# Performance work log

Hardware: AMD Instinct MI355X
Metric: run time of the kernel (lower is better)

Reference implementation:

```python
import jax, jax.numpy as jnp
import numpy as np

N, E, B = 100000, 1600000, 64
IN, HID, OUT, ED = 64, 128, 128, 2
K, ALPHA = 16, 0.1
LN_EPS = 1e-5


def setup_inputs() -> dict:
    key = jax.random.key(0)
    ks = jax.random.split(key, 24)
    def gl(k, shape, fan_in):
        return jax.random.uniform(k, shape, jnp.float32, -1.0, 1.0) / np.sqrt(fan_in)
    inp = {
        "x": jax.random.normal(ks[0], (N, IN), jnp.float32),
        "edge_index": jax.random.randint(ks[1], (2, E), 0, N, jnp.int64),
        "batch": jnp.sort(jax.random.randint(ks[2], (N,), 0, B, jnp.int64)),
        "edge_attr": jax.random.normal(ks[3], (E, ED), jnp.float32),
        # conv1: edge lin (ED->IN) + mlp (IN->HID->HID)
        "We1": gl(ks[4], (ED, IN), ED), "be1": jnp.zeros((IN,)),
        "W1a": gl(ks[5], (IN, HID), IN), "b1a": jnp.zeros((HID,)),
        "W1b": gl(ks[6], (HID, HID), HID), "b1b": jnp.zeros((HID,)),
        "g1": jnp.ones((HID,)), "bn1": jnp.zeros((HID,)),
        # conv2: edge lin (ED->HID) + mlp (HID->OUT->OUT)
        "We2": gl(ks[7], (ED, HID), ED), "be2": jnp.zeros((HID,)),
        "W2a": gl(ks[8], (HID, OUT), HID), "b2a": jnp.zeros((OUT,)),
        "W2b": gl(ks[9], (OUT, OUT), OUT), "b2b": jnp.zeros((OUT,)),
        "g2": jnp.ones((OUT,)), "bn2": jnp.zeros((OUT,)),
        # gate nn (OUT -> OUT//2 -> 1)
        "Wg1": gl(ks[10], (OUT, OUT // 2), OUT), "bg1": jnp.zeros((OUT // 2,)),
        "Wg2": gl(ks[11], (OUT // 2, 1), OUT // 2), "bg2": jnp.zeros((1,)),
    }
    return inp


def _gelu(x):
    return jax.nn.gelu(x, approximate=False)


def _layernorm(x, g, b):
    mu = jnp.mean(x, axis=-1, keepdims=True)
    var = jnp.mean(jnp.square(x - mu), axis=-1, keepdims=True)
    return (x - mu) * jax.lax.rsqrt(var + LN_EPS) * g + b


def _gine(x, src, dst, edge_attr, We, be, W1, b1, W2, b2):
    # message: ReLU(x_j + lin(edge_attr)), aggregated by sum at dst; eps=0
    m = jax.nn.relu(x[src] + edge_attr @ We + be)          # [E, d]
    agg = jax.ops.segment_sum(m, dst, num_segments=N)      # [N, d]
    h = x + agg
    return _gelu(h @ W1 + b1) @ W2 + b2


def _appnp(x, src, dst):
    # gcn_norm with self-loops: deg_i = 1 + in-degree
    deg = jax.ops.segment_sum(jnp.ones((E,), x.dtype), dst, num_segments=N) + 1.0
    dis = jax.lax.rsqrt(deg)
    w = dis[src] * dis[dst]            # [E]
    selfw = 1.0 / deg                  # [N]
    def step(i, h):
        prop = jax.ops.segment_sum(w[:, None] * h[src], dst, num_segments=N) \
               + selfw[:, None] * h
        return (1.0 - ALPHA) * prop + ALPHA * x
    return jax.lax.fori_loop(0, K, step, x)


def reference(x, edge_index, batch, edge_attr,
              We1, be1, W1a, b1a, W1b, b1b, g1, bn1,
              We2, be2, W2a, b2a, W2b, b2b, g2, bn2,
              Wg1, bg1, Wg2, bg2):
    src, dst = edge_index[0], edge_index[1]
    h = _gine(x, src, dst, edge_attr, We1, be1, W1a, b1a, W1b, b1b)
    h = _layernorm(_gelu(h), g1, bn1)
    # dropout is identity in eval
    h = _gine(h, src, dst, edge_attr, We2, be2, W2a, b2a, W2b, b2b)
    h = _layernorm(h, g2, bn2)
    h = _appnp(h, src, dst)
    # attentional aggregation: per-graph softmax over gate scores
    gate = (_gelu(h @ Wg1 + bg1) @ Wg2 + bg2)[:, 0]        # [N]
    m = jax.ops.segment_max(gate, batch, num_segments=B)    # [B]
    e = jnp.exp(gate - m[batch])
    s = jax.ops.segment_sum(e, batch, num_segments=B)
    a = e / s[batch]
    g = jax.ops.segment_sum(a[:, None] * h, batch, num_segments=B)  # [B, OUT]
    return h, g
```

## Files before the change

kernel.cpp:

```cpp
#include <hip/hip_runtime.h>
#include <math.h>

#define N_NODES 100000
#define N_EDGES 1600000
#define N_B 64
#define D_IN 64
#define D_HID 128
#define D_OUT 128
#define K_ITER 16
#define LN_EPS 1e-5f

typedef short s8v __attribute__((ext_vector_type(8)));
typedef float f4v __attribute__((ext_vector_type(4)));

__device__ __forceinline__ float gelu_f(float x) {
    return 0.5f * x * (1.0f + erff(0.70710678118654752440f * x));
}

__device__ __forceinline__ float ubx(unsigned u) { return __uint_as_float(u << 16); }
__device__ __forceinline__ float uby(unsigned u) { return __uint_as_float(u & 0xffff0000u); }

__device__ __forceinline__ unsigned short bf_rne(float x) {
    unsigned u = __float_as_uint(x);
    u += 0x7fffu + ((u >> 16) & 1u);
    return (unsigned short)(u >> 16);
}
__device__ __forceinline__ float bf_f(unsigned short s) {
    return __uint_as_float(((unsigned)s) << 16);
}
__device__ __forceinline__ unsigned pack_bf2(float a, float b) {
    return (unsigned)bf_rne(a) | (((unsigned)bf_rne(b)) << 16);
}


__global__ __launch_bounds__(256) void hist_kernel(const int* __restrict__ dst, int* __restrict__ counts) {
    int e = blockIdx.x * 256 + threadIdx.x;
    if (e < N_EDGES) atomicAdd(&counts[dst[e]], 1);
}

__global__ __launch_bounds__(256) void deg_kernel(const int* __restrict__ counts,
                                                  float* __restrict__ dis, float* __restrict__ selfw) {
    int i = blockIdx.x * 256 + threadIdx.x;
    if (i < N_NODES) {
        float d = (float)(counts[i] + 1);
        dis[i] = 1.0f / sqrtf(d);
        selfw[i] = 1.0f / d;
    }
}

__global__ __launch_bounds__(1024) void scan1(const int* __restrict__ counts, int* __restrict__ rp,
                                              int* __restrict__ bsum) {
    __shared__ int tmp[1024];
    int t = threadIdx.x;
    int idx = blockIdx.x * 1024 + t;
    int v = (idx < N_NODES) ? counts[idx] : 0;
    tmp[t] = v;
    __syncthreads();
    for (int o = 1; o < 1024; o <<= 1) {
        int add = (t >= o) ? tmp[t - o] : 0;
        __syncthreads();
        tmp[t] += add;
        __syncthreads();
    }
    if (idx < N_NODES) rp[idx] = tmp[t] - v;
    if (t == 1023) bsum[blockIdx.x] = tmp[t];
}

__global__ void scan2(int* bsum, int nb) {
    if (threadIdx.x == 0 && blockIdx.x == 0) {
        int acc = 0;
        for (int i = 0; i < nb; i++) { int v = bsum[i]; bsum[i] = acc; acc += v; }
    }
}

__global__ __launch_bounds__(1024) void scan3(int* __restrict__ rp, const int* __restrict__ bsum,
                                              int* __restrict__ cursor) {
    int t = threadIdx.x;
    int idx = blockIdx.x * 1024 + t;
    if (idx < N_NODES) {
        int v = rp[idx] + bsum[blockIdx.x];
        rp[idx] = v;
        cursor[idx] = v;
    }
    if (idx == 0) rp[N_NODES] = N_EDGES;
}

__global__ __launch_bounds__(256) void scatter_kernel(const int* __restrict__ src, const int* __restrict__ dst,
                                                      const float* __restrict__ ea, const float* __restrict__ dis,
                                                      int* __restrict__ cursor, int2* __restrict__ esw,
                                                      float2* __restrict__ eea) {
    int e = blockIdx.x * 256 + threadIdx.x;
    if (e >= N_EDGES) return;
    int s = src[e], d = dst[e];
    int pos = atomicAdd(&cursor[d], 1);
    int2 sw;
    sw.x = s;
    sw.y = __float_as_int(dis[s] * dis[d]);
    esw[pos] = sw;
    float2 e2;
    e2.x = ea[e * 2];
    e2.y = ea[e * 2 + 1];
    eea[pos] = e2;
}


__global__ __launch_bounds__(256) void conv1_gather(const float* __restrict__ x, const int* __restrict__ rp,
                                                    const int2* __restrict__ esw, const float2* __restrict__ eea,
                                                    const float* __restrict__ We1, const float* __restrict__ be1,
                                                    float* __restrict__ out) {
    int gw = (blockIdx.x * 256 + threadIdx.x) >> 6;
    if (gw >= N_NODES) return;
    int lane = threadIdx.x & 63;
    float w0 = We1[lane], w1 = We1[64 + lane], bb = be1[lane];
    float acc = x[(size_t)gw * 64 + lane];
    int j = rp[gw], s1 = rp[gw + 1];
    for (; j + 4 <= s1; j += 4) {
        int2 e0 = esw[j], e1 = esw[j + 1], e2 = esw[j + 2], e3 = esw[j + 3];
        float2 a0 = eea[j], a1 = eea[j + 1], a2 = eea[j + 2], a3 = eea[j + 3];
        float v0 = x[(size_t)e0.x * 64 + lane];
        float v1 = x[(size_t)e1.x * 64 + lane];
        float v2 = x[(size_t)e2.x * 64 + lane];
        float v3 = x[(size_t)e3.x * 64 + lane];
        acc += fmaxf(v0 + a0.x * w0 + a0.y * w1 + bb, 0.0f);
        acc += fmaxf(v1 + a1.x * w0 + a1.y * w1 + bb, 0.0f);
        acc += fmaxf(v2 + a2.x * w0 + a2.y * w1 + bb, 0.0f);
        acc += fmaxf(v3 + a3.x * w0 + a3.y * w1 + bb, 0.0f);
    }
    for (; j < s1; j++) {
        int2 e = esw[j];
        float2 a = eea[j];
        float v = x[(size_t)e.x * 64 + lane];
        acc += fmaxf(v + a.x * w0 + a.y * w1 + bb, 0.0f);
    }
    out[(size_t)gw * 64 + lane] = acc;
}

__global__ __launch_bounds__(256) void conv2_gather(const float* __restrict__ h1f, const unsigned* __restrict__ h1b,
                                                    const int* __restrict__ rp,
                                                    const int2* __restrict__ esw, const float2* __restrict__ eea,
                                                    const float* __restrict__ We2, const float* __restrict__ be2,
                                                    float* __restrict__ out) {
    int gw = (blockIdx.x * 256 + threadIdx.x) >> 6;
    if (gw >= N_NODES) return;
    int lane = threadIdx.x & 63;
    int f0 = lane * 2;
    float w00 = We2[f0], w01 = We2[f0 + 1];
    float w10 = We2[128 + f0], w11 = We2[128 + f0 + 1];
    float b0 = be2[f0], b1 = be2[f0 + 1];
    float2 hc = ((const float2*)h1f)[(size_t)gw * 64 + lane];
    float a0 = hc.x, a1 = hc.y;
    int j = rp[gw], s1 = rp[gw + 1];
    for (; j + 8 <= s1; j += 8) {
        int2 e0 = esw[j], e1 = esw[j + 1], e2 = esw[j + 2], e3 = esw[j + 3];
        int2 e4 = esw[j + 4], e5 = esw[j + 5], e6 = esw[j + 6], e7 = esw[j + 7];
        float2 q0 = eea[j], q1 = eea[j + 1], q2 = eea[j + 2], q3 = eea[j + 3];
        float2 q4 = eea[j + 4], q5 = eea[j + 5], q6 = eea[j + 6], q7 = eea[j + 7];
        unsigned v0 = h1b[(size_t)e0.x * 64 + lane];
        unsigned v1 = h1b[(size_t)e1.x * 64 + lane];
        unsigned v2 = h1b[(size_t)e2.x * 64 + lane];
        unsigned v3 = h1b[(size_t)e3.x * 64 + lane];
        unsigned v4 = h1b[(size_t)e4.x * 64 + lane];
        unsigned v5 = h1b[(size_t)e5.x * 64 + lane];
        unsigned v6 = h1b[(size_t)e6.x * 64 + lane];
        unsigned v7 = h1b[(size_t)e7.x * 64 + lane];
        a0 += fmaxf(ubx(v0) + q0.x * w00 + q0.y * w10 + b0, 0.0f);
        a1 += fmaxf(uby(v0) + q0.x * w01 + q0.y * w11 + b1, 0.0f);
        a0 += fmaxf(ubx(v1) + q1.x * w00 + q1.y * w10 + b0, 0.0f);
        a1 += fmaxf(uby(v1) + q1.x * w01 + q1.y * w11 + b1, 0.0f);
        a0 += fmaxf(ubx(v2) + q2.x * w00 + q2.y * w10 + b0, 0.0f);
        a1 += fmaxf(uby(v2) + q2.x * w01 + q2.y * w11 + b1, 0.0f);
        a0 += fmaxf(ubx(v3) + q3.x * w00 + q3.y * w10 + b0, 0.0f);
        a1 += fmaxf(uby(v3) + q3.x * w01 + q3.y * w11 + b1, 0.0f);
        a0 += fmaxf(ubx(v4) + q4.x * w00 + q4.y * w10 + b0, 0.0f);
        a1 += fmaxf(uby(v4) + q4.x * w01 + q4.y * w11 + b1, 0.0f);
        a0 += fmaxf(ubx(v5) + q5.x * w00 + q5.y * w10 + b0, 0.0f);
        a1 += fmaxf(uby(v5) + q5.x * w01 + q5.y * w11 + b1, 0.0f);
        a0 += fmaxf(ubx(v6) + q6.x * w00 + q6.y * w10 + b0, 0.0f);
        a1 += fmaxf(uby(v6) + q6.x * w01 + q6.y * w11 + b1, 0.0f);
        a0 += fmaxf(ubx(v7) + q7.x * w00 + q7.y * w10 + b0, 0.0f);
        a1 += fmaxf(uby(v7) + q7.x * w01 + q7.y * w11 + b1, 0.0f);
    }
    for (; j < s1; j++) {
        int2 e = esw[j];
        float2 q = eea[j];
        unsigned v = h1b[(size_t)e.x * 64 + lane];
        a0 += fmaxf(ubx(v) + q.x * w00 + q.y * w10 + b0, 0.0f);
        a1 += fmaxf(uby(v) + q.x * w01 + q.y * w11 + b1, 0.0f);
    }
    out[(size_t)gw * 128 + f0] = a0;
    out[(size_t)gw * 128 + f0 + 1] = a1;
}


template <int Kd, bool GELU, bool LN, int OMODE>
__global__ __launch_bounds__(256) void mlp_mfma(const float* __restrict__ A, const float* __restrict__ W,
                                                const float* __restrict__ bias, const float* __restrict__ g,
                                                const float* __restrict__ bn, float* __restrict__ outf,
                                                unsigned short* __restrict__ outb) {
    __shared__ unsigned short sHi[8192];
    __shared__ unsigned short sLo[8192];
    int wave = threadIdx.x >> 6, lane = threadIdx.x & 63;
    int quad = lane >> 4, n = lane & 15;
    int rowA = blockIdx.x * 64 + wave * 16 + n;
    int rowAc = (rowA < N_NODES) ? rowA : 0;

    f4v acc[8];
    #pragma unroll
    for (int t = 0; t < 8; t++) acc[t] = (f4v){0.f, 0.f, 0.f, 0.f};

    for (int ph = 0; ph < Kd / 64; ph++) {
        __syncthreads();
        for (int idx = threadIdx.x; idx < 8192; idx += 256) {
            int k = idx >> 7, c = idx & 127;
            float v = W[(size_t)(ph * 64 + k) * 128 + c];
            unsigned short hi = bf_rne(v);
            unsigned short lo = bf_rne(v - bf_f(hi));
            int kk = k >> 5, q = (k >> 3) & 3, j = k & 7, t = c >> 4, nn = c & 15;
            int lidx = ((((kk * 4 + q) * 8 + t) * 16 + nn) << 3) + j;
            sHi[lidx] = hi;
            sLo[lidx] = lo;
        }
        __syncthreads();
        #pragma unroll
        for (int kk = 0; kk < 2; kk++) {
            int k0 = ph * 64 + kk * 32 + quad * 8;
            const float4* ap = (const float4*)(A + (size_t)rowAc * Kd + k0);
            float4 a0 = ap[0], a1 = ap[1];
            float av[8] = {a0.x, a0.y, a0.z, a0.w, a1.x, a1.y, a1.z, a1.w};
            s8v ahi, alo;
            #pragma unroll
            for (int j = 0; j < 8; j++) {
                unsigned short h = bf_rne(av[j]);
                ahi[j] = (short)h;
                alo[j] = (short)bf_rne(av[j] - bf_f(h));
            }
            int base = ((kk * 4 + quad) * 8) * 128;
            #pragma unroll
            for (int t = 0; t < 8; t++) {
                s8v bhi = *(const s8v*)&sHi[base + ((t * 16 + n) << 3)];
                s8v blo = *(const s8v*)&sLo[base + ((t * 16 + n) << 3)];
                acc[t] = __builtin_amdgcn_mfma_f32_16x16x32_bf16(ahi, bhi, acc[t], 0, 0, 0);
                acc[t] = __builtin_amdgcn_mfma_f32_16x16x32_bf16(ahi, blo, acc[t], 0, 0, 0);
                acc[t] = __builtin_amdgcn_mfma_f32_16x16x32_bf16(alo, bhi, acc[t], 0, 0, 0);
            }
        }
    }

    float bcol[8], gcol[8], bncol[8];
    #pragma unroll
    for (int t = 0; t < 8; t++) {
        bcol[t] = bias[t * 16 + n];
        if (LN) { gcol[t] = g[t * 16 + n]; bncol[t] = bn[t * 16 + n]; }
    }
    #pragma unroll
    for (int r = 0; r < 4; r++) {
        int row = blockIdx.x * 64 + wave * 16 + quad * 4 + r;
        float v[8];
        #pragma unroll
        for (int t = 0; t < 8; t++) {
            float x = acc[t][r] + bcol[t];
            v[t] = GELU ? gelu_f(x) : x;
        }
        if (LN) {
            float s = 0.f, q2 = 0.f;
            #pragma unroll
            for (int t = 0; t < 8; t++) { s += v[t]; q2 += v[t] * v[t]; }
            #pragma unroll
            for (int m = 1; m <= 8; m <<= 1) {
                s += __shfl_xor(s, m, 64);
                q2 += __shfl_xor(q2, m, 64);
            }
            float mu = s * (1.0f / 128.0f);
            float rs = rsqrtf(q2 * (1.0f / 128.0f) - mu * mu + LN_EPS);
            #pragma unroll
            for (int t = 0; t < 8; t++) v[t] = (v[t] - mu) * rs * gcol[t] + bncol[t];
        }
        if (row < N_NODES) {
            #pragma unroll
            for (int t = 0; t < 8; t++) {
                if (OMODE != 2) outf[(size_t)row * 128 + t * 16 + n] = v[t];
                if (OMODE >= 1) outb[(size_t)row * 128 + t * 16 + n] = bf_rne(v[t]);
            }
        }
    }
}


__global__ __launch_bounds__(256) void gate_mfma(const float* __restrict__ h, const float* __restrict__ Wg1,
                                                 const float* __restrict__ bg1, const float* __restrict__ Wg2,
                                                 const float* __restrict__ bg2, float* __restrict__ gate) {
    __shared__ unsigned short sHi[8192];
    __shared__ unsigned short sLo[8192];
    int wave = threadIdx.x >> 6, lane = threadIdx.x & 63;
    int quad = lane >> 4, n = lane & 15;
    for (int idx = threadIdx.x; idx < 8192; idx += 256) {
        int k = idx >> 6, c = idx & 63;
        float v = Wg1[k * 64 + c];
        unsigned short hi = bf_rne(v);
        unsigned short lo = bf_rne(v - bf_f(hi));
        int kk = k >> 5, q = (k >> 3) & 3, j = k & 7, t = c >> 4, nn = c & 15;
        int lidx = ((((kk * 4 + q) * 4 + t) * 16 + nn) << 3) + j;
        sHi[lidx] = hi;
        sLo[lidx] = lo;
    }
    __syncthreads();
    int rowA = blockIdx.x * 64 + wave * 16 + n;
    int rowAc = (rowA < N_NODES) ? rowA : 0;
    f4v acc[4];
    #pragma unroll
    for (int t = 0; t < 4; t++) acc[t] = (f4v){0.f, 0.f, 0.f, 0.f};
    #pragma unroll
    for (int kk = 0; kk < 4; kk++) {
        const float4* ap = (const float4*)(h + (size_t)rowAc * 128 + kk * 32 + quad * 8);
        float4 a0 = ap[0], a1 = ap[1];
        float av[8] = {a0.x, a0.y, a0.z, a0.w, a1.x, a1.y, a1.z, a1.w};
        s8v ahi, alo;
        #pragma unroll
        for (int j = 0; j < 8; j++) {
            unsigned short hh = bf_rne(av[j]);
            ahi[j] = (short)hh;
            alo[j] = (short)bf_rne(av[j] - bf_f(hh));
        }
        int base = ((kk * 4 + quad) * 4) * 128;
        #pragma unroll
        for (int t = 0; t < 4; t++) {
            s8v bhi = *(const s8v*)&sHi[base + ((t * 16 + n) << 3)];
            s8v blo = *(const s8v*)&sLo[base + ((t * 16 + n) << 3)];
            acc[t] = __builtin_amdgcn_mfma_f32_16x16x32_bf16(ahi, bhi, acc[t], 0, 0, 0);
            acc[t] = __builtin_amdgcn_mfma_f32_16x16x32_bf16(ahi, blo, acc[t], 0, 0, 0);
            acc[t] = __builtin_amdgcn_mfma_f32_16x16x32_bf16(alo, bhi, acc[t], 0, 0, 0);
        }
    }
    float b2 = bg2[0];
    float bb[4], vv[4];
    #pragma unroll
    for (int t = 0; t < 4; t++) { bb[t] = bg1[t * 16 + n]; vv[t] = Wg2[t * 16 + n]; }
    #pragma unroll
    for (int r = 0; r < 4; r++) {
        int row = blockIdx.x * 64 + wave * 16 + quad * 4 + r;
        float val = 0.f;
        #pragma unroll
        for (int t = 0; t < 4; t++) val += gelu_f(acc[t][r] + bb[t]) * vv[t];
        #pragma unroll
        for (int m = 1; m <= 8; m <<= 1) val += __shfl_xor(val, m, 64);
        if (n == 0 && row < N_NODES) gate[row] = val + b2;
    }
}


template <bool LAST>
__global__ __launch_bounds__(256) void appnp_step_bf(const unsigned* __restrict__ hin,
                                                     const unsigned* __restrict__ anchor,
                                                     unsigned* __restrict__ hout, float2* __restrict__ houtf,
                                                     const int* __restrict__ rp, const int2* __restrict__ esw,
                                                     const float* __restrict__ selfw) {
    int gw = (blockIdx.x * 256 + threadIdx.x) >> 6;
    if (gw >= N_NODES) return;
    int lane = threadIdx.x & 63;
    size_t idx = (size_t)gw * 64 + lane;
    float swi = selfw[gw];
    unsigned hcp = hin[idx];
    float ax = swi * ubx(hcp), ay = swi * uby(hcp);
    int j = rp[gw], s1 = rp[gw + 1];
    for (; j + 8 <= s1; j += 8) {
        int2 e0 = esw[j], e1 = esw[j + 1], e2 = esw[j + 2], e3 = esw[j + 3];
        int2 e4 = esw[j + 4], e5 = esw[j + 5], e6 = esw[j + 6], e7 = esw[j + 7];
        unsigned v0 = hin[(size_t)e0.x * 64 + lane];
        unsigned v1 = hin[(size_t)e1.x * 64 + lane];
        unsigned v2 = hin[(size_t)e2.x * 64 + lane];
        unsigned v3 = hin[(size_t)e3.x * 64 + lane];
        unsigned v4 = hin[(size_t)e4.x * 64 + lane];
        unsigned v5 = hin[(size_t)e5.x * 64 + lane];
        unsigned v6 = hin[(size_t)e6.x * 64 + lane];
        unsigned v7 = hin[(size_t)e7.x * 64 + lane];
        float w0 = __int_as_float(e0.y), w1 = __int_as_float(e1.y);
        float w2 = __int_as_float(e2.y), w3 = __int_as_float(e3.y);
        float w4 = __int_as_float(e4.y), w5 = __int_as_float(e5.y);
        float w6 = __int_as_float(e6.y), w7 = __int_as_float(e7.y);
        ax = fmaf(w0, ubx(v0), ax); ay = fmaf(w0, uby(v0), ay);
        ax = fmaf(w1, ubx(v1), ax); ay = fmaf(w1, uby(v1), ay);
        ax = fmaf(w2, ubx(v2), ax); ay = fmaf(w2, uby(v2), ay);
        ax = fmaf(w3, ubx(v3), ax); ay = fmaf(w3, uby(v3), ay);
        ax = fmaf(w4, ubx(v4), ax); ay = fmaf(w4, uby(v4), ay);
        ax = fmaf(w5, ubx(v5), ax); ay = fmaf(w5, uby(v5), ay);
        ax = fmaf(w6, ubx(v6), ax); ay = fmaf(w6, uby(v6), ay);
        ax = fmaf(w7, ubx(v7), ax); ay = fmaf(w7, uby(v7), ay);
    }
    for (; j + 4 <= s1; j += 4) {
        int2 e0 = esw[j], e1 = esw[j + 1], e2 = esw[j + 2], e3 = esw[j + 3];
        unsigned v0 = hin[(size_t)e0.x * 64 + lane];
        unsigned v1 = hin[(size_t)e1.x * 64 + lane];
        unsigned v2 = hin[(size_t)e2.x * 64 + lane];
        unsigned v3 = hin[(size_t)e3.x * 64 + lane];
        float w0 = __int_as_float(e0.y), w1 = __int_as_float(e1.y);
        float w2 = __int_as_float(e2.y), w3 = __int_as_float(e3.y);
        ax = fmaf(w0, ubx(v0), ax); ay = fmaf(w0, uby(v0), ay);
        ax = fmaf(w1, ubx(v1), ax); ay = fmaf(w1, uby(v1), ay);
        ax = fmaf(w2, ubx(v2), ax); ay = fmaf(w2, uby(v2), ay);
        ax = fmaf(w3, ubx(v3), ax); ay = fmaf(w3, uby(v3), ay);
    }
    for (; j < s1; j++) {
        int2 e = esw[j];
        unsigned v = hin[(size_t)e.x * 64 + lane];
        float w = __int_as_float(e.y);
        ax = fmaf(w, ubx(v), ax); ay = fmaf(w, uby(v), ay);
    }
    unsigned ancp = anchor[idx];
    float ox = 0.9f * ax + 0.1f * ubx(ancp);
    float oy = 0.9f * ay + 0.1f * uby(ancp);
    if (LAST) {
        float2 o; o.x = ox; o.y = oy;
        houtf[idx] = o;
    } else {
        hout[idx] = pack_bf2(ox, oy);
    }
}


__global__ void seg_begin(const int* __restrict__ batch, int* __restrict__ gbeg) {
    int b = threadIdx.x;
    if (b > N_B) return;
    if (b == N_B) { gbeg[N_B] = N_NODES; return; }
    int lo = 0, hi = N_NODES;
    while (lo < hi) {
        int mid = (lo + hi) >> 1;
        if (batch[mid] < b) lo = mid + 1; else hi = mid;
    }
    gbeg[b] = lo;
}

__global__ __launch_bounds__(256) void seg_max(const float* __restrict__ gate, const int* __restrict__ gbeg,
                                               float* __restrict__ gmax) {
    int b = blockIdx.x;
    int s = gbeg[b], e = gbeg[b + 1];
    float m = -INFINITY;
    for (int i = s + threadIdx.x; i < e; i += 256) m = fmaxf(m, gate[i]);
    for (int o = 32; o > 0; o >>= 1) m = fmaxf(m, __shfl_xor(m, o, 64));
    __shared__ float red[4];
    if ((threadIdx.x & 63) == 0) red[threadIdx.x >> 6] = m;
    __syncthreads();
    if (threadIdx.x == 0) gmax[b] = fmaxf(fmaxf(red[0], red[1]), fmaxf(red[2], red[3]));
}

__global__ __launch_bounds__(256) void seg_sum(const float* __restrict__ gate, const int* __restrict__ gbeg,
                                               const float* __restrict__ gmax, float* __restrict__ gsum) {
    int b = blockIdx.x;
    int s = gbeg[b], e = gbeg[b + 1];
    float m = gmax[b];
    float acc = 0.0f;
    for (int i = s + threadIdx.x; i < e; i += 256) acc += expf(gate[i] - m);
    for (int o = 32; o > 0; o >>= 1) acc += __shfl_xor(acc, o, 64);
    __shared__ float red[4];
    if ((threadIdx.x & 63) == 0) red[threadIdx.x >> 6] = acc;
    __syncthreads();
    if (threadIdx.x == 0) gsum[b] = red[0] + red[1] + red[2] + red[3];
}

__global__ __launch_bounds__(512) void seg_pool(const float* __restrict__ h, const float* __restrict__ gate,
                                                const int* __restrict__ gbeg, const float* __restrict__ gmax,
                                                const float* __restrict__ gsum, float* __restrict__ gout) {
    int b = blockIdx.x >> 3, slice = blockIdx.x & 7;
    int team = threadIdx.x >> 7;
    int f = threadIdx.x & 127;
    int s = gbeg[b], e = gbeg[b + 1];
    float m = gmax[b];
    float inv = (e > s) ? 1.0f / gsum[b] : 0.0f;
    float acc = 0.0f;
    for (int i = s + slice * 4 + team; i < e; i += 32) {
        float a = expf(gate[i] - m) * inv;
        acc = fmaf(a, h[(size_t)i * 128 + f], acc);
    }
    __shared__ float red[4][128];
    red[team][f] = acc;
    __syncthreads();
    if (team == 0) {
        float v = red[0][f] + red[1][f] + red[2][f] + red[3][f];
        atomicAdd(&gout[b * 128 + f], v);
    }
}


extern "C" void kernel_launch(void* const* d_in, const int* in_sizes, int n_in,
                              void* d_out, int out_size, void* d_ws, size_t ws_size,
                              hipStream_t stream) {
    const float* x     = (const float*)d_in[0];
    const int*   ei    = (const int*)d_in[1];
    const int*   batch = (const int*)d_in[2];
    const float* ea    = (const float*)d_in[3];
    const float* We1 = (const float*)d_in[4];
    const float* be1 = (const float*)d_in[5];
    const float* W1a = (const float*)d_in[6];
    const float* b1a = (const float*)d_in[7];
    const float* W1b = (const float*)d_in[8];
    const float* b1b = (const float*)d_in[9];
    const float* g1  = (const float*)d_in[10];
    const float* bn1 = (const float*)d_in[11];
    const float* We2 = (const float*)d_in[12];
    const float* be2 = (const float*)d_in[13];
    const float* W2a = (const float*)d_in[14];
    const float* b2a = (const float*)d_in[15];
    const float* W2b = (const float*)d_in[16];
    const float* b2b = (const float*)d_in[17];
    const float* g2  = (const float*)d_in[18];
    const float* bn2 = (const float*)d_in[19];
    const float* Wg1 = (const float*)d_in[20];
    const float* bg1 = (const float*)d_in[21];
    const float* Wg2 = (const float*)d_in[22];
    const float* bg2 = (const float*)d_in[23];

    float* outH = (float*)d_out;
    float* outG = outH + (size_t)N_NODES * 128;

    char* w = (char*)d_ws;
    auto carve = [&](size_t bytes) {
        void* p = (void*)w;
        w += ((bytes + 255) / 256) * 256;
        return p;
    };
    float*  bufB   = (float*)carve((size_t)N_NODES * 128 * 4);
    float*  bufC   = (float*)carve((size_t)N_NODES * 128 * 4);
    int2*   esw    = (int2*)carve((size_t)N_EDGES * 8);
    float2* eea    = (float2*)carve((size_t)N_EDGES * 8);
    int*    counts = (int*)carve((size_t)N_NODES * 4);
    int*    rp     = (int*)carve((size_t)(N_NODES + 1) * 4);
    int*    cursor = (int*)carve((size_t)N_NODES * 4);
    float*  dis    = (float*)carve((size_t)N_NODES * 4);
    float*  selfw  = (float*)carve((size_t)N_NODES * 4);
    float*  gate   = (float*)carve((size_t)N_NODES * 4);
    int*    bsum   = (int*)carve(128 * 4);
    float*  gmax   = (float*)carve(N_B * 4);
    float*  gsum   = (float*)carve(N_B * 4);
    int*    gbeg   = (int*)carve((N_B + 1) * 4);

    const int* src = ei;
    const int* dst = ei + N_EDGES;

    const int NB_SCAN = (N_NODES + 1023) / 1024;
    const int EB = (N_EDGES + 255) / 256;
    const int NBLK = (N_NODES + 255) / 256;
    const int WBLK = (N_NODES + 3) / 4;
    const int MBLK = (N_NODES + 63) / 64;

    hipMemsetAsync(counts, 0, (size_t)N_NODES * 4, stream);
    hist_kernel<<<EB, 256, 0, stream>>>(dst, counts);
    deg_kernel<<<NBLK, 256, 0, stream>>>(counts, dis, selfw);
    scan1<<<NB_SCAN, 1024, 0, stream>>>(counts, rp, bsum);
    scan2<<<1, 64, 0, stream>>>(bsum, NB_SCAN);
    scan3<<<NB_SCAN, 1024, 0, stream>>>(rp, bsum, cursor);
    scatter_kernel<<<EB, 256, 0, stream>>>(src, dst, ea, dis, cursor, esw, eea);

    unsigned short* h1bf  = (unsigned short*)bufC;
    unsigned* ancU  = (unsigned*)bufC;
    unsigned* pingA = ancU + (size_t)N_NODES * 64;
    unsigned* pingB = (unsigned*)bufB;

    conv1_gather<<<WBLK, 256, 0, stream>>>(x, rp, esw, eea, We1, be1, bufB);
    mlp_mfma<64, true, false, 0><<<MBLK, 256, 0, stream>>>(bufB, W1a, b1a, nullptr, nullptr, outH, nullptr);
    mlp_mfma<128, true, true, 1><<<MBLK, 256, 0, stream>>>(outH, W1b, b1b, g1, bn1, bufB, h1bf);

    conv2_gather<<<WBLK, 256, 0, stream>>>(bufB, (const unsigned*)h1bf, rp, esw, eea, We2, be2, outH);
    mlp_mfma<128, true, false, 0><<<MBLK, 256, 0, stream>>>(outH, W2a, b2a, nullptr, nullptr, bufB, nullptr);
    mlp_mfma<128, false, true, 2><<<MBLK, 256, 0, stream>>>(bufB, W2b, b2b, g2, bn2, nullptr, (unsigned short*)ancU);

    const unsigned* cur = ancU;
    for (int k = 1; k <= K_ITER - 1; k++) {
        unsigned* dstbuf = (k & 1) ? pingA : pingB;
        appnp_step_bf<false><<<WBLK, 256, 0, stream>>>(cur, ancU, dstbuf, nullptr, rp, esw, selfw);
        cur = dstbuf;
    }
    appnp_step_bf<true><<<WBLK, 256, 0, stream>>>(cur, ancU, nullptr, (float2*)outH, rp, esw, selfw);

    gate_mfma<<<MBLK, 256, 0, stream>>>(outH, Wg1, bg1, Wg2, bg2, gate);
    seg_begin<<<1, 128, 0, stream>>>(batch, gbeg);
    seg_max<<<N_B, 256, 0, stream>>>(gate, gbeg, gmax);
    seg_sum<<<N_B, 256, 0, stream>>>(gate, gbeg, gmax, gsum);
    hipMemsetAsync(outG, 0, (size_t)N_B * 128 * 4, stream);
    seg_pool<<<N_B * 8, 512, 0, stream>>>(outH, gate, gbeg, gmax, gsum, outG);
}
```

Baseline: 1.812 ms.

## Pack edge records as int4 and drop stored weights from APPNP edge stream

```diff
diff --git a/kernel.cpp b/kernel.cpp
--- a/kernel.cpp
+++ b/kernel.cpp
@@ -86,26 +86,29 @@
 }
 
 __global__ __launch_bounds__(256) void scatter_kernel(const int* __restrict__ src, const int* __restrict__ dst,
-                                                      const float* __restrict__ ea, const float* __restrict__ dis,
-                                                      int* __restrict__ cursor, int2* __restrict__ esw,
-                                                      float2* __restrict__ eea) {
+                                                      const float* __restrict__ ea,
+                                                      int* __restrict__ cursor, int4* __restrict__ edata) {
     int e = blockIdx.x * 256 + threadIdx.x;
     if (e >= N_EDGES) return;
     int s = src[e], d = dst[e];
     int pos = atomicAdd(&cursor[d], 1);
-    int2 sw;
-    sw.x = s;
-    sw.y = __float_as_int(dis[s] * dis[d]);
-    esw[pos] = sw;
-    float2 e2;
-    e2.x = ea[e * 2];
-    e2.y = ea[e * 2 + 1];
-    eea[pos] = e2;
+    float2 e2 = ((const float2*)ea)[e];
+    int4 v;
+    v.x = s;
+    v.y = __float_as_int(e2.x);
+    v.z = __float_as_int(e2.y);
+    v.w = 0;
+    edata[pos] = v;
+}
+
+__global__ __launch_bounds__(256) void split_kernel(const int4* __restrict__ edata, int* __restrict__ esrc) {
+    int e = blockIdx.x * 256 + threadIdx.x;
+    if (e < N_EDGES) esrc[e] = edata[e].x;
 }
 
 
 __global__ __launch_bounds__(256) void conv1_gather(const float* __restrict__ x, const int* __restrict__ rp,
-                                                    const int2* __restrict__ esw, const float2* __restrict__ eea,
+                                                    const int4* __restrict__ edata,
                                                     const float* __restrict__ We1, const float* __restrict__ be1,
                                                     float* __restrict__ out) {
     int gw = (blockIdx.x * 256 + threadIdx.x) >> 6;
@@ -113,31 +116,38 @@
     int lane = threadIdx.x & 63;
     float w0 = We1[lane], w1 = We1[64 + lane], bb = be1[lane];
     float acc = x[(size_t)gw * 64 + lane];
-    int j = rp[gw], s1 = rp[gw + 1];
-    for (; j + 4 <= s1; j += 4) {
-        int2 e0 = esw[j], e1 = esw[j + 1], e2 = esw[j + 2], e3 = esw[j + 3];
-        float2 a0 = eea[j], a1 = eea[j + 1], a2 = eea[j + 2], a3 = eea[j + 3];
+    int j = rp[gw], jend = rp[gw + 1];
+    for (; j + 8 <= jend; j += 8) {
+        int4 e0 = edata[j], e1 = edata[j + 1], e2 = edata[j + 2], e3 = edata[j + 3];
+        int4 e4 = edata[j + 4], e5 = edata[j + 5], e6 = edata[j + 6], e7 = edata[j + 7];
         float v0 = x[(size_t)e0.x * 64 + lane];
         float v1 = x[(size_t)e1.x * 64 + lane];
         float v2 = x[(size_t)e2.x * 64 + lane];
         float v3 = x[(size_t)e3.x * 64 + lane];
-        acc += fmaxf(v0 + a0.x * w0 + a0.y * w1 + bb, 0.0f);
-        acc += fmaxf(v1 + a1.x * w0 + a1.y * w1 + bb, 0.0f);
-        acc += fmaxf(v2 + a2.x * w0 + a2.y * w1 + bb, 0.0f);
-        acc += fmaxf(v3 + a3.x * w0 + a3.y * w1 + bb, 0.0f);
-    }
-    for (; j < s1; j++) {
-        int2 e = esw[j];
-        float2 a = eea[j];
+        float v4 = x[(size_t)e4.x * 64 + lane];
+        float v5 = x[(size_t)e5.x * 64 + lane];
+        float v6 = x[(size_t)e6.x * 64 + lane];
+        float v7 = x[(size_t)e7.x * 64 + lane];
+        acc += fmaxf(v0 + __int_as_float(e0.y) * w0 + __int_as_float(e0.z) * w1 + bb, 0.0f);
+        acc += fmaxf(v1 + __int_as_float(e1.y) * w0 + __int_as_float(e1.z) * w1 + bb, 0.0f);
+        acc += fmaxf(v2 + __int_as_float(e2.y) * w0 + __int_as_float(e2.z) * w1 + bb, 0.0f);
+        acc += fmaxf(v3 + __int_as_float(e3.y) * w0 + __int_as_float(e3.z) * w1 + bb, 0.0f);
+        acc += fmaxf(v4 + __int_as_float(e4.y) * w0 + __int_as_float(e4.z) * w1 + bb, 0.0f);
+        acc += fmaxf(v5 + __int_as_float(e5.y) * w0 + __int_as_float(e5.z) * w1 + bb, 0.0f);
+        acc += fmaxf(v6 + __int_as_float(e6.y) * w0 + __int_as_float(e6.z) * w1 + bb, 0.0f);
+        acc += fmaxf(v7 + __int_as_float(e7.y) * w0 + __int_as_float(e7.z) * w1 + bb, 0.0f);
+    }
+    for (; j < jend; j++) {
+        int4 e = edata[j];
         float v = x[(size_t)e.x * 64 + lane];
-        acc += fmaxf(v + a.x * w0 + a.y * w1 + bb, 0.0f);
+        acc += fmaxf(v + __int_as_float(e.y) * w0 + __int_as_float(e.z) * w1 + bb, 0.0f);
     }
     out[(size_t)gw * 64 + lane] = acc;
 }
 
 __global__ __launch_bounds__(256) void conv2_gather(const float* __restrict__ h1f, const unsigned* __restrict__ h1b,
                                                     const int* __restrict__ rp,
-                                                    const int2* __restrict__ esw, const float2* __restrict__ eea,
+                                                    const int4* __restrict__ edata,
                                                     const float* __restrict__ We2, const float* __restrict__ be2,
                                                     float* __restrict__ out) {
     int gw = (blockIdx.x * 256 + threadIdx.x) >> 6;
@@ -149,12 +159,10 @@
     float b0 = be2[f0], b1 = be2[f0 + 1];
     float2 hc = ((const float2*)h1f)[(size_t)gw * 64 + lane];
     float a0 = hc.x, a1 = hc.y;
-    int j = rp[gw], s1 = rp[gw + 1];
-    for (; j + 8 <= s1; j += 8) {
-        int2 e0 = esw[j], e1 = esw[j + 1], e2 = esw[j + 2], e3 = esw[j + 3];
-        int2 e4 = esw[j + 4], e5 = esw[j + 5], e6 = esw[j + 6], e7 = esw[j + 7];
-        float2 q0 = eea[j], q1 = eea[j + 1], q2 = eea[j + 2], q3 = eea[j + 3];
-        float2 q4 = eea[j + 4], q5 = eea[j + 5], q6 = eea[j + 6], q7 = eea[j + 7];
+    int j = rp[gw], jend = rp[gw + 1];
+    for (; j + 8 <= jend; j += 8) {
+        int4 e0 = edata[j], e1 = edata[j + 1], e2 = edata[j + 2], e3 = edata[j + 3];
+        int4 e4 = edata[j + 4], e5 = edata[j + 5], e6 = edata[j + 6], e7 = edata[j + 7];
         unsigned v0 = h1b[(size_t)e0.x * 64 + lane];
         unsigned v1 = h1b[(size_t)e1.x * 64 + lane];
         unsigned v2 = h1b[(size_t)e2.x * 64 + lane];
@@ -163,29 +171,28 @@
         unsigned v5 = h1b[(size_t)e5.x * 64 + lane];
         unsigned v6 = h1b[(size_t)e6.x * 64 + lane];
         unsigned v7 = h1b[(size_t)e7.x * 64 + lane];
-        a0 += fmaxf(ubx(v0) + q0.x * w00 + q0.y * w10 + b0, 0.0f);
-        a1 += fmaxf(uby(v0) + q0.x * w01 + q0.y * w11 + b1, 0.0f);
-        a0 += fmaxf(ubx(v1) + q1.x * w00 + q1.y * w10 + b0, 0.0f);
-        a1 += fmaxf(uby(v1) + q1.x * w01 + q1.y * w11 + b1, 0.0f);
-        a0 += fmaxf(ubx(v2) + q2.x * w00 + q2.y * w10 + b0, 0.0f);
-        a1 += fmaxf(uby(v2) + q2.x * w01 + q2.y * w11 + b1, 0.0f);
-        a0 += fmaxf(ubx(v3) + q3.x * w00 + q3.y * w10 + b0, 0.0f);
-        a1 += fmaxf(uby(v3) + q3.x * w01 + q3.y * w11 + b1, 0.0f);
-        a0 += fmaxf(ubx(v4) + q4.x * w00 + q4.y * w10 + b0, 0.0f);
-        a1 += fmaxf(uby(v4) + q4.x * w01 + q4.y * w11 + b1, 0.0f);
-        a0 += fmaxf(ubx(v5) + q5.x * w00 + q5.y * w10 + b0, 0.0f);
-        a1 += fmaxf(uby(v5) + q5.x * w01 + q5.y * w11 + b1, 0.0f);
-        a0 += fmaxf(ubx(v6) + q6.x * w00 + q6.y * w10 + b0, 0.0f);
-        a1 += fmaxf(uby(v6) + q6.x * w01 + q6.y * w11 + b1, 0.0f);
-        a0 += fmaxf(ubx(v7) + q7.x * w00 + q7.y * w10 + b0, 0.0f);
-        a1 += fmaxf(uby(v7) + q7.x * w01 + q7.y * w11 + b1, 0.0f);
-    }
-    for (; j < s1; j++) {
-        int2 e = esw[j];
-        float2 q = eea[j];
+        a0 += fmaxf(ubx(v0) + __int_as_float(e0.y) * w00 + __int_as_float(e0.z) * w10 + b0, 0.0f);
+        a1 += fmaxf(uby(v0) + __int_as_float(e0.y) * w01 + __int_as_float(e0.z) * w11 + b1, 0.0f);
+        a0 += fmaxf(ubx(v1) + __int_as_float(e1.y) * w00 + __int_as_float(e1.z) * w10 + b0, 0.0f);
+        a1 += fmaxf(uby(v1) + __int_as_float(e1.y) * w01 + __int_as_float(e1.z) * w11 + b1, 0.0f);
+        a0 += fmaxf(ubx(v2) + __int_as_float(e2.y) * w00 + __int_as_float(e2.z) * w10 + b0, 0.0f);
+        a1 += fmaxf(uby(v2) + __int_as_float(e2.y) * w01 + __int_as_float(e2.z) * w11 + b1, 0.0f);
+        a0 += fmaxf(ubx(v3) + __int_as_float(e3.y) * w00 + __int_as_float(e3.z) * w10 + b0, 0.0f);
+        a1 += fmaxf(uby(v3) + __int_as_float(e3.y) * w01 + __int_as_float(e3.z) * w11 + b1, 0.0f);
+        a0 += fmaxf(ubx(v4) + __int_as_float(e4.y) * w00 + __int_as_float(e4.z) * w10 + b0, 0.0f);
+        a1 += fmaxf(uby(v4) + __int_as_float(e4.y) * w01 + __int_as_float(e4.z) * w11 + b1, 0.0f);
+        a0 += fmaxf(ubx(v5) + __int_as_float(e5.y) * w00 + __int_as_float(e5.z) * w10 + b0, 0.0f);
+        a1 += fmaxf(uby(v5) + __int_as_float(e5.y) * w01 + __int_as_float(e5.z) * w11 + b1, 0.0f);
+        a0 += fmaxf(ubx(v6) + __int_as_float(e6.y) * w00 + __int_as_float(e6.z) * w10 + b0, 0.0f);
+        a1 += fmaxf(uby(v6) + __int_as_float(e6.y) * w01 + __int_as_float(e6.z) * w11 + b1, 0.0f);
+        a0 += fmaxf(ubx(v7) + __int_as_float(e7.y) * w00 + __int_as_float(e7.z) * w10 + b0, 0.0f);
+        a1 += fmaxf(uby(v7) + __int_as_float(e7.y) * w01 + __int_as_float(e7.z) * w11 + b1, 0.0f);
+    }
+    for (; j < jend; j++) {
+        int4 e = edata[j];
         unsigned v = h1b[(size_t)e.x * 64 + lane];
-        a0 += fmaxf(ubx(v) + q.x * w00 + q.y * w10 + b0, 0.0f);
-        a1 += fmaxf(uby(v) + q.x * w01 + q.y * w11 + b1, 0.0f);
+        a0 += fmaxf(ubx(v) + __int_as_float(e.y) * w00 + __int_as_float(e.z) * w10 + b0, 0.0f);
+        a1 += fmaxf(uby(v) + __int_as_float(e.y) * w01 + __int_as_float(e.z) * w11 + b1, 0.0f);
     }
     out[(size_t)gw * 128 + f0] = a0;
     out[(size_t)gw * 128 + f0 + 1] = a1;
@@ -352,31 +359,31 @@
 __global__ __launch_bounds__(256) void appnp_step_bf(const unsigned* __restrict__ hin,
                                                      const unsigned* __restrict__ anchor,
                                                      unsigned* __restrict__ hout, float2* __restrict__ houtf,
-                                                     const int* __restrict__ rp, const int2* __restrict__ esw,
+                                                     const int* __restrict__ rp, const int* __restrict__ esrc,
+                                                     const float* __restrict__ dis,
                                                      const float* __restrict__ selfw) {
     int gw = (blockIdx.x * 256 + threadIdx.x) >> 6;
     if (gw >= N_NODES) return;
     int lane = threadIdx.x & 63;
     size_t idx = (size_t)gw * 64 + lane;
     float swi = selfw[gw];
+    float wd = dis[gw];
     unsigned hcp = hin[idx];
     float ax = swi * ubx(hcp), ay = swi * uby(hcp);
-    int j = rp[gw], s1 = rp[gw + 1];
-    for (; j + 8 <= s1; j += 8) {
-        int2 e0 = esw[j], e1 = esw[j + 1], e2 = esw[j + 2], e3 = esw[j + 3];
-        int2 e4 = esw[j + 4], e5 = esw[j + 5], e6 = esw[j + 6], e7 = esw[j + 7];
-        unsigned v0 = hin[(size_t)e0.x * 64 + lane];
-        unsigned v1 = hin[(size_t)e1.x * 64 + lane];
-        unsigned v2 = hin[(size_t)e2.x * 64 + lane];
-        unsigned v3 = hin[(size_t)e3.x * 64 + lane];
-        unsigned v4 = hin[(size_t)e4.x * 64 + lane];
-        unsigned v5 = hin[(size_t)e5.x * 64 + lane];
-        unsigned v6 = hin[(size_t)e6.x * 64 + lane];
-        unsigned v7 = hin[(size_t)e7.x * 64 + lane];
-        float w0 = __int_as_float(e0.y), w1 = __int_as_float(e1.y);
-        float w2 = __int_as_float(e2.y), w3 = __int_as_float(e3.y);
-        float w4 = __int_as_float(e4.y), w5 = __int_as_float(e5.y);
-        float w6 = __int_as_float(e6.y), w7 = __int_as_float(e7.y);
+    int j = rp[gw], jend = rp[gw + 1];
+    for (; j + 8 <= jend; j += 8) {
+        int s0 = esrc[j],     s1 = esrc[j + 1], s2 = esrc[j + 2], s3 = esrc[j + 3];
+        int s4 = esrc[j + 4], s5 = esrc[j + 5], s6 = esrc[j + 6], s7 = esrc[j + 7];
+        unsigned v0 = hin[(size_t)s0 * 64 + lane];
+        unsigned v1 = hin[(size_t)s1 * 64 + lane];
+        unsigned v2 = hin[(size_t)s2 * 64 + lane];
+        unsigned v3 = hin[(size_t)s3 * 64 + lane];
+        unsigned v4 = hin[(size_t)s4 * 64 + lane];
+        unsigned v5 = hin[(size_t)s5 * 64 + lane];
+        unsigned v6 = hin[(size_t)s6 * 64 + lane];
+        unsigned v7 = hin[(size_t)s7 * 64 + lane];
+        float w0 = dis[s0] * wd, w1 = dis[s1] * wd, w2 = dis[s2] * wd, w3 = dis[s3] * wd;
+        float w4 = dis[s4] * wd, w5 = dis[s5] * wd, w6 = dis[s6] * wd, w7 = dis[s7] * wd;
         ax = fmaf(w0, ubx(v0), ax); ay = fmaf(w0, uby(v0), ay);
         ax = fmaf(w1, ubx(v1), ax); ay = fmaf(w1, uby(v1), ay);
         ax = fmaf(w2, ubx(v2), ax); ay = fmaf(w2, uby(v2), ay);
@@ -386,23 +393,22 @@
         ax = fmaf(w6, ubx(v6), ax); ay = fmaf(w6, uby(v6), ay);
         ax = fmaf(w7, ubx(v7), ax); ay = fmaf(w7, uby(v7), ay);
     }
-    for (; j + 4 <= s1; j += 4) {
-        int2 e0 = esw[j], e1 = esw[j + 1], e2 = esw[j + 2], e3 = esw[j + 3];
-        unsigned v0 = hin[(size_t)e0.x * 64 + lane];
-        unsigned v1 = hin[(size_t)e1.x * 64 + lane];
-        unsigned v2 = hin[(size_t)e2.x * 64 + lane];
-        unsigned v3 = hin[(size_t)e3.x * 64 + lane];
-        float w0 = __int_as_float(e0.y), w1 = __int_as_float(e1.y);
-        float w2 = __int_as_float(e2.y), w3 = __int_as_float(e3.y);
+    for (; j + 4 <= jend; j += 4) {
+        int s0 = esrc[j], s1 = esrc[j + 1], s2 = esrc[j + 2], s3 = esrc[j + 3];
+        unsigned v0 = hin[(size_t)s0 * 64 + lane];
+        unsigned v1 = hin[(size_t)s1 * 64 + lane];
+        unsigned v2 = hin[(size_t)s2 * 64 + lane];
+        unsigned v3 = hin[(size_t)s3 * 64 + lane];
+        float w0 = dis[s0] * wd, w1 = dis[s1] * wd, w2 = dis[s2] * wd, w3 = dis[s3] * wd;
         ax = fmaf(w0, ubx(v0), ax); ay = fmaf(w0, uby(v0), ay);
         ax = fmaf(w1, ubx(v1), ax); ay = fmaf(w1, uby(v1), ay);
         ax = fmaf(w2, ubx(v2), ax); ay = fmaf(w2, uby(v2), ay);
         ax = fmaf(w3, ubx(v3), ax); ay = fmaf(w3, uby(v3), ay);
     }
-    for (; j < s1; j++) {
-        int2 e = esw[j];
-        unsigned v = hin[(size_t)e.x * 64 + lane];
-        float w = __int_as_float(e.y);
+    for (; j < jend; j++) {
+        int s = esrc[j];
+        unsigned v = hin[(size_t)s * 64 + lane];
+        float w = dis[s] * wd;
         ax = fmaf(w, ubx(v), ax); ay = fmaf(w, uby(v), ay);
     }
     unsigned ancp = anchor[idx];
@@ -519,8 +525,7 @@
     };
     float*  bufB   = (float*)carve((size_t)N_NODES * 128 * 4);
     float*  bufC   = (float*)carve((size_t)N_NODES * 128 * 4);
-    int2*   esw    = (int2*)carve((size_t)N_EDGES * 8);
-    float2* eea    = (float2*)carve((size_t)N_EDGES * 8);
+    int4*   edata  = (int4*)carve((size_t)N_EDGES * 16);
     int*    counts = (int*)carve((size_t)N_NODES * 4);
     int*    rp     = (int*)carve((size_t)(N_NODES + 1) * 4);
     int*    cursor = (int*)carve((size_t)N_NODES * 4);
@@ -547,28 +552,31 @@
     scan1<<<NB_SCAN, 1024, 0, stream>>>(counts, rp, bsum);
     scan2<<<1, 64, 0, stream>>>(bsum, NB_SCAN);
     scan3<<<NB_SCAN, 1024, 0, stream>>>(rp, bsum, cursor);
-    scatter_kernel<<<EB, 256, 0, stream>>>(src, dst, ea, dis, cursor, esw, eea);
+    scatter_kernel<<<EB, 256, 0, stream>>>(src, dst, ea, cursor, edata);
 
     unsigned short* h1bf  = (unsigned short*)bufC;
     unsigned* ancU  = (unsigned*)bufC;
     unsigned* pingA = ancU + (size_t)N_NODES * 64;
     unsigned* pingB = (unsigned*)bufB;
-
-    conv1_gather<<<WBLK, 256, 0, stream>>>(x, rp, esw, eea, We1, be1, bufB);
+    int*      esrc  = (int*)(bufB + (size_t)N_NODES * 64);
+
+    conv1_gather<<<WBLK, 256, 0, stream>>>(x, rp, edata, We1, be1, bufB);
     mlp_mfma<64, true, false, 0><<<MBLK, 256, 0, stream>>>(bufB, W1a, b1a, nullptr, nullptr, outH, nullptr);
     mlp_mfma<128, true, true, 1><<<MBLK, 256, 0, stream>>>(outH, W1b, b1b, g1, bn1, bufB, h1bf);
 
-    conv2_gather<<<WBLK, 256, 0, stream>>>(bufB, (const unsigned*)h1bf, rp, esw, eea, We2, be2, outH);
+    conv2_gather<<<WBLK, 256, 0, stream>>>(bufB, (const unsigned*)h1bf, rp, edata, We2, be2, outH);
     mlp_mfma<128, true, false, 0><<<MBLK, 256, 0, stream>>>(outH, W2a, b2a, nullptr, nullptr, bufB, nullptr);
     mlp_mfma<128, false, true, 2><<<MBLK, 256, 0, stream>>>(bufB, W2b, b2b, g2, bn2, nullptr, (unsigned short*)ancU);
+
+    split_kernel<<<EB, 256, 0, stream>>>(edata, esrc);
 
     const unsigned* cur = ancU;
     for (int k = 1; k <= K_ITER - 1; k++) {
         unsigned* dstbuf = (k & 1) ? pingA : pingB;
-        appnp_step_bf<false><<<WBLK, 256, 0, stream>>>(cur, ancU, dstbuf, nullptr, rp, esw, selfw);
+        appnp_step_bf<false><<<WBLK, 256, 0, stream>>>(cur, ancU, dstbuf, nullptr, rp, esrc, dis, selfw);
         cur = dstbuf;
     }
-    appnp_step_bf<true><<<WBLK, 256, 0, stream>>>(cur, ancU, nullptr, (float2*)outH, rp, esw, selfw);
+    appnp_step_bf<true><<<WBLK, 256, 0, stream>>>(cur, ancU, nullptr, (float2*)outH, rp, esrc, dis, selfw);
 
     gate_mfma<<<MBLK, 256, 0, stream>>>(outH, Wg1, bg1, Wg2, bg2, gate);
     seg_begin<<<1, 128, 0, stream>>>(batch, gbeg);
```

Measured after the change: 1.860 ms. 1.03x slower.
